# Optimization experiments

Measured on AMD Instinct MI355X. Metric: run time of the kernel, lower is better.

Reference implementation:

```python
import jax, jax.numpy as jnp
import numpy as np

N_NODES = 50000
N_EDGES = 800000
N_GRAPHS = 256
D_FEAT = 96
HIDDEN = 32


def setup_inputs() -> dict:
    key = jax.random.key(0)
    ks = jax.random.split(key, 8)
    x = jax.random.normal(ks[0], (N_NODES, D_FEAT), dtype=jnp.float32)
    edge_index = jax.random.randint(ks[1], (2, N_EDGES), 0, N_NODES, dtype=jnp.int64)
    batch = jnp.sort(jax.random.randint(ks[2], (N_NODES,), 0, N_GRAPHS, dtype=jnp.int64))
    W1 = jax.random.normal(ks[3], (D_FEAT, HIDDEN), dtype=jnp.float32) * 0.05
    b1 = jnp.zeros((HIDDEN,), dtype=jnp.float32)
    W2 = jax.random.normal(ks[4], (HIDDEN, HIDDEN), dtype=jnp.float32) * 0.05
    b2 = jnp.zeros((HIDDEN,), dtype=jnp.float32)
    Wc = jax.random.normal(ks[5], (HIDDEN, 2), dtype=jnp.float32) * 0.05
    bc = jnp.zeros((2,), dtype=jnp.float32)
    return {"x": x, "edge_index": edge_index, "batch": batch,
            "W1": W1, "b1": b1, "W2": W2, "b2": b2, "Wc": Wc, "bc": bc}


def reference(x, edge_index, batch, W1, b1, W2, b2, Wc, bc):
    src, dst = edge_index[0], edge_index[1]
    # GIN aggregation (eps=0): h_i = x_i + sum_{j -> i} x_j, scatter-add over edges
    agg = jax.ops.segment_sum(x[src], dst, num_segments=N_NODES)
    h = agg + x
    # 2-layer MLP inside GINConv
    h = jnp.maximum(h @ W1 + b1, 0.0) @ W2 + b2
    # outer ReLU (F.relu in forward)
    h = jnp.maximum(h, 0.0)
    # global mean pool per graph
    sums = jax.ops.segment_sum(h, batch, num_segments=N_GRAPHS)          # [G, H]
    counts = jax.ops.segment_sum(jnp.ones((N_NODES,), h.dtype), batch,
                                 num_segments=N_GRAPHS)                   # [G]
    pooled = sums / jnp.maximum(counts, 1.0)[:, None]
    return pooled @ Wc + bc  # [G, 2]
```

## Files before the change

### kernel.cpp

```cpp
#include <hip/hip_runtime.h>
#include <hip/hip_fp16.h>

#define N_NODES 50000
#define N_EDGES 800000
#define N_GRAPHS 256
#define D_FEAT 96
#define HIDDEN 32

#define NB 196
#define PB 500
#define PCHUNK 1600
#define SEGCAP 32
#define NLOAD 16
#define GWIN 16
#define LCAP 6400
#define XT 64
#define XBLK 782
#define XS_STRIDE 97
#define DUMMY_NODE N_NODES

__global__ void __launch_bounds__(256)
k_front(const float* __restrict__ x, const float* __restrict__ W1,
        __half* __restrict__ y16,
        const int* __restrict__ src, const int* __restrict__ dst,
        unsigned int* __restrict__ binned, unsigned short* __restrict__ cnt,
        float* __restrict__ sums, float* __restrict__ counts) {
    __shared__ __align__(16) char smem[26656];
    int blk = blockIdx.x;
    int tid = threadIdx.x;
    if (blk < PB) {
        int* hcur = (int*)smem;
        for (int i = tid; i < NB; i += 256) hcur[i] = 0;
        __syncthreads();

        int e0 = blk * PCHUNK, e1 = e0 + PCHUNK;
        for (int it = 0; it < PCHUNK; it += 1024) {
            int e = e0 + it + tid * 4;
            if (e < e1) {
                int4 s4 = *(const int4*)&src[e];
                int4 d4 = *(const int4*)&dst[e];
                unsigned w0 = (unsigned)s4.x | ((unsigned)(d4.x & 255) << 16);
                unsigned w1 = (unsigned)s4.y | ((unsigned)(d4.y & 255) << 16);
                unsigned w2 = (unsigned)s4.z | ((unsigned)(d4.z & 255) << 16);
                unsigned w3 = (unsigned)s4.w | ((unsigned)(d4.w & 255) << 16);
                int b0 = d4.x >> 8, b1 = d4.y >> 8, b2 = d4.z >> 8, b3 = d4.w >> 8;
                int p0 = atomicAdd(&hcur[b0], 1);
                int p1 = atomicAdd(&hcur[b1], 1);
                int p2 = atomicAdd(&hcur[b2], 1);
                int p3 = atomicAdd(&hcur[b3], 1);
                if (p0 < SEGCAP) binned[((size_t)b0 * PB + blk) * SEGCAP + p0] = w0;
                if (p1 < SEGCAP) binned[((size_t)b1 * PB + blk) * SEGCAP + p1] = w1;
                if (p2 < SEGCAP) binned[((size_t)b2 * PB + blk) * SEGCAP + p2] = w2;
                if (p3 < SEGCAP) binned[((size_t)b3 * PB + blk) * SEGCAP + p3] = w3;
            }
        }
        __syncthreads();

        for (int i = tid; i < NB; i += 256) {
            int c = hcur[i]; if (c > SEGCAP) c = SEGCAP;
            cnt[i * PB + blk] = (unsigned short)c;
        }
    } else {
        float* xs = (float*)smem;
        int xb = blk - PB;
        int n0 = xb * XT;
        int nn = N_NODES - n0; if (nn > XT) nn = XT;

        int gid = xb * 256 + tid;
        if (gid < N_GRAPHS * HIDDEN) sums[gid] = 0.f;
        if (gid < N_GRAPHS) counts[gid] = 0.f;
        if (xb == 0 && tid < HIDDEN)
            y16[(size_t)DUMMY_NODE * HIDDEN + tid] = __float2half(0.f);

        const float4* xsrc = (const float4*)(x + (size_t)n0 * D_FEAT);
        int nf4 = nn * (D_FEAT / 4);
        for (int idx = tid; idx < nf4; idx += 256) {
            int ln = (idx * 2731) >> 16;
            int k4 = idx - ln * 24;
            float4 v = xsrc[idx];
            float* dp = &xs[ln * XS_STRIDE + k4 * 4];
            dp[0] = v.x; dp[1] = v.y; dp[2] = v.z; dp[3] = v.w;
        }
        __syncthreads();

        int lane = tid & 63;
        int f0 = (tid >> 6) << 3;
        f0 = __builtin_amdgcn_readfirstlane(f0);

        if (lane < nn) {
            const float* xr = &xs[lane * XS_STRIDE];
            const float4* W1v = (const float4*)W1;
            float acc[8];
#pragma unroll
            for (int j = 0; j < 8; ++j) acc[j] = 0.f;
#pragma unroll
            for (int k = 0; k < D_FEAT; ++k) {
                float xv = xr[k];
                float4 wa = W1v[k * 8 + (f0 >> 2)];
                float4 wb = W1v[k * 8 + (f0 >> 2) + 1];
                acc[0] = fmaf(xv, wa.x, acc[0]);
                acc[1] = fmaf(xv, wa.y, acc[1]);
                acc[2] = fmaf(xv, wa.z, acc[2]);
                acc[3] = fmaf(xv, wa.w, acc[3]);
                acc[4] = fmaf(xv, wb.x, acc[4]);
                acc[5] = fmaf(xv, wb.y, acc[5]);
                acc[6] = fmaf(xv, wb.z, acc[6]);
                acc[7] = fmaf(xv, wb.w, acc[7]);
            }
            __half2 h01 = __floats2half2_rn(acc[0], acc[1]);
            __half2 h23 = __floats2half2_rn(acc[2], acc[3]);
            __half2 h45 = __floats2half2_rn(acc[4], acc[5]);
            __half2 h67 = __floats2half2_rn(acc[6], acc[7]);
            float4 pack;
            pack.x = __uint_as_float(*(const unsigned*)&h01);
            pack.y = __uint_as_float(*(const unsigned*)&h23);
            pack.z = __uint_as_float(*(const unsigned*)&h45);
            pack.w = __uint_as_float(*(const unsigned*)&h67);
            *(float4*)&y16[(size_t)(n0 + lane) * HIDDEN + f0] = pack;
        }
    }
}

__global__ void __launch_bounds__(1024)
k_agg(const unsigned int* __restrict__ binned, const unsigned short* __restrict__ cnt,
      const __half* __restrict__ y16, const int* __restrict__ batch,
      const float* __restrict__ b1, const float* __restrict__ W2,
      const float* __restrict__ b2,
      float* __restrict__ sums, float* __restrict__ counts) {
    __shared__ unsigned int list[LCAP];
    __shared__ unsigned short list2[LCAP];
    __shared__ unsigned int sA[512], sB[512];
    __shared__ unsigned short cs[PB];
    __shared__ unsigned int sOfs[PB];
    __shared__ unsigned int ncnt[256];
    __shared__ unsigned int offs[257];
    __shared__ unsigned int cur[256];
    __shared__ float w2s[HIDDEN * HIDDEN];
    __shared__ float accs[GWIN * HIDDEN];
    __shared__ float cntsl[GWIN];

    int tid = threadIdx.x;
    int bin = blockIdx.x;
    if (tid < 256) ncnt[tid] = 0;
    w2s[tid] = W2[tid];
    if (tid < GWIN * HIDDEN) accs[tid] = 0.f;
    if (tid < GWIN) cntsl[tid] = 0.f;
    if (tid < 512) {
        unsigned c = (tid < PB) ? (unsigned)cnt[bin * PB + tid] : 0u;
        if (tid < PB) cs[tid] = (unsigned short)c;
        sA[tid] = c;
    }

    const unsigned int* ebase = binned + (size_t)bin * PB * SEGCAP;
    unsigned u[NLOAD];
#pragma unroll
    for (int j = 0; j < NLOAD; ++j)
        u[j] = ebase[tid + j * 1024];
    __syncthreads();

    unsigned *ps = sA, *pd = sB;
    for (int d = 1; d < 512; d <<= 1) {
        if (tid < 512) { unsigned v = ps[tid]; if (tid >= d) v += ps[tid - d]; pd[tid] = v; }
        __syncthreads();
        unsigned* t = ps; ps = pd; pd = t;
    }
    if (tid < PB) sOfs[tid] = tid ? ps[tid - 1] : 0u;
    int ecount = (int)ps[PB - 1];
    if (ecount > LCAP) ecount = LCAP;
    __syncthreads();

#pragma unroll
    for (int j = 0; j < NLOAD; ++j) {
        int idx = tid + j * 1024;
        if (idx < PB * SEGCAP) {
            int s = idx >> 5;
            int i = idx & 31;
            if (i < (int)cs[s]) {
                unsigned pos = sOfs[s] + i;
                if (pos < LCAP) list[pos] = u[j];
            }
        }
    }
    __syncthreads();

    for (int e = tid; e < ecount; e += 1024)
        atomicAdd(&ncnt[list[e] >> 16], 1u);
    __syncthreads();

    if (tid < 256) sA[tid] = (ncnt[tid] + 7u) & ~7u;
    __syncthreads();
    ps = sA; pd = sB;
    for (int d = 1; d < 256; d <<= 1) {
        if (tid < 256) { unsigned v = ps[tid]; if (tid >= d) v += ps[tid - d]; pd[tid] = v; }
        __syncthreads();
        unsigned* t = ps; ps = pd; pd = t;
    }
    if (tid < 256) {
        offs[tid + 1] = ps[tid];
        cur[tid] = tid ? ps[tid - 1] : 0u;
    }
    if (tid == 0) offs[0] = 0;
    __syncthreads();

    for (int e = tid; e < ecount; e += 1024) {
        unsigned p = list[e];
        unsigned pos = atomicAdd(&cur[p >> 16], 1u);
        if (pos < LCAP) list2[pos] = (unsigned short)(p & 0xFFFFu);
    }
    __syncthreads();
    if (tid < 256) {
        unsigned i0 = cur[tid], i1 = offs[tid + 1];
        for (unsigned i = i0; i < i1 && i < LCAP; ++i)
            list2[i] = (unsigned short)DUMMY_NODE;
    }
    __syncthreads();

    int node0 = bin << 8;
    int nn = N_NODES - node0; if (nn > 256) nn = 256;
    int g = tid >> 5;
    int f = tid & 31;
    int gfirst = batch[node0];

    for (int ln = g * 8; ln < g * 8 + 8; ++ln) {
        if (ln >= nn) break;
        int node = node0 + ln;
        float acc = __half2float(y16[(size_t)node * HIDDEN + f]);
        int j = offs[ln], jend = offs[ln + 1];
        for (; j < jend; j += 8) {
            ushort4 qa = *(const ushort4*)&list2[j];
            ushort4 qb = *(const ushort4*)&list2[j + 4];
            float a0 = __half2float(y16[(size_t)qa.x * HIDDEN + f]);
            float a1 = __half2float(y16[(size_t)qa.y * HIDDEN + f]);
            float a2 = __half2float(y16[(size_t)qa.z * HIDDEN + f]);
            float a3 = __half2float(y16[(size_t)qa.w * HIDDEN + f]);
            float a4 = __half2float(y16[(size_t)qb.x * HIDDEN + f]);
            float a5 = __half2float(y16[(size_t)qb.y * HIDDEN + f]);
            float a6 = __half2float(y16[(size_t)qb.z * HIDDEN + f]);
            float a7 = __half2float(y16[(size_t)qb.w * HIDDEN + f]);
            acc += ((a0 + a1) + (a2 + a3)) + ((a4 + a5) + (a6 + a7));
        }

        float h1 = fmaxf(acc + b1[f], 0.f);
        float h2 = b2[f];
#pragma unroll
        for (int k = 0; k < HIDDEN; ++k)
            h2 = fmaf(__shfl(h1, k, 32), w2s[k * HIDDEN + f], h2);
        float h = fmaxf(h2, 0.f);

        int gr = batch[node];
        int b = gr - gfirst;
        if (b < GWIN) {
            atomicAdd(&accs[b * HIDDEN + f], h);
            if (f == 0) atomicAdd(&cntsl[b], 1.f);
        } else {
            atomicAdd(&sums[(size_t)gr * HIDDEN + f], h);
            if (f == 0) atomicAdd(&counts[gr], 1.f);
        }
    }
    __syncthreads();

    for (int i = tid; i < GWIN * HIDDEN; i += 1024) {
        float v = accs[i];
        if (v != 0.f) atomicAdd(&sums[(size_t)gfirst * HIDDEN + i], v);
    }
    if (tid < GWIN) {
        float c = cntsl[tid];
        if (c != 0.f) atomicAdd(&counts[gfirst + tid], c);
    }
}

__global__ void k_out(const float* __restrict__ sums, const float* __restrict__ counts,
                      const float* __restrict__ Wc, const float* __restrict__ bc,
                      float* __restrict__ out) {
    int g = threadIdx.x;
    if (g >= N_GRAPHS) return;
    float inv = 1.f / fmaxf(counts[g], 1.f);
    float o0 = bc[0], o1 = bc[1];
#pragma unroll
    for (int k = 0; k < HIDDEN; ++k) {
        float p = sums[(size_t)g * HIDDEN + k] * inv;
        o0 = fmaf(p, Wc[k * 2 + 0], o0);
        o1 = fmaf(p, Wc[k * 2 + 1], o1);
    }
    out[g * 2 + 0] = o0;
    out[g * 2 + 1] = o1;
}

extern "C" void kernel_launch(void* const* d_in, const int* in_sizes, int n_in,
                              void* d_out, int out_size, void* d_ws, size_t ws_size,
                              hipStream_t stream) {
    const float* x     = (const float*)d_in[0];
    const int*   ei    = (const int*)d_in[1];
    const int*   batch = (const int*)d_in[2];
    const float* W1    = (const float*)d_in[3];
    const float* b1    = (const float*)d_in[4];
    const float* W2    = (const float*)d_in[5];
    const float* b2    = (const float*)d_in[6];
    const float* Wc    = (const float*)d_in[7];
    const float* bc    = (const float*)d_in[8];
    float* out = (float*)d_out;

    char* ws = (char*)d_ws;
    float*          sums   = (float*)ws;
    float*          counts = (float*)(ws + 32768);
    unsigned short* cnt    = (unsigned short*)(ws + 33792);
    unsigned int*   binned = (unsigned int*)(ws + 229792);
    __half*         y16    = (__half*)(ws + 12773792);

    k_front<<<PB + XBLK, 256, 0, stream>>>(
        x, W1, y16, ei, ei + N_EDGES, binned, cnt, sums, counts);

    k_agg<<<NB, 1024, 0, stream>>>(binned, cnt, y16, batch,
                                   b1, W2, b2, sums, counts);

    k_out<<<1, 256, 0, stream>>>(sums, counts, Wc, bc, out);
}
```

Before: 127.0 us.

## Shrink aggregation bins to 64 nodes and drop intermediate edge compaction

Bins are shrunk from 256 to 64 destination nodes, so the aggregation kernel runs 782 blocks instead of 196. That fills more compute units and cuts per-block work and synchronisation. The old two-stage compaction (block-wide scan into a 32-bit list, then re-binning by node) is replaced by counting and scattering straight from registers, with a single wavefront shuffle scan over 64 node counts. The cost is a binned buffer twice the size (with SEGCAP 16) and more per-bin count entries, which adds memory traffic in both kernels.

```diff
diff --git a/kernel.cpp b/kernel.cpp
--- a/kernel.cpp
+++ b/kernel.cpp
@@ -7,13 +7,14 @@
 #define D_FEAT 96
 #define HIDDEN 32
 
-#define NB 196
+#define NB 782
+#define BN 64
 #define PB 500
 #define PCHUNK 1600
-#define SEGCAP 32
-#define NLOAD 16
-#define GWIN 16
-#define LCAP 6400
+#define SEGCAP 16
+#define NLOAD 8
+#define GWIN 4
+#define LCAP2 2048
 #define XT 64
 #define XBLK 782
 #define XS_STRIDE 97
@@ -43,7 +44,7 @@
                 unsigned w1 = (unsigned)s4.y | ((unsigned)(d4.y & 255) << 16);
                 unsigned w2 = (unsigned)s4.z | ((unsigned)(d4.z & 255) << 16);
                 unsigned w3 = (unsigned)s4.w | ((unsigned)(d4.w & 255) << 16);
-                int b0 = d4.x >> 8, b1 = d4.y >> 8, b2 = d4.z >> 8, b3 = d4.w >> 8;
+                int b0 = d4.x >> 6, b1 = d4.y >> 6, b2 = d4.z >> 6, b3 = d4.w >> 6;
                 int p0 = atomicAdd(&hcur[b0], 1);
                 int p1 = atomicAdd(&hcur[b1], 1);
                 int p2 = atomicAdd(&hcur[b2], 1);
@@ -127,105 +128,89 @@
       const float* __restrict__ b1, const float* __restrict__ W2,
       const float* __restrict__ b2,
       float* __restrict__ sums, float* __restrict__ counts) {
-    __shared__ unsigned int list[LCAP];
-    __shared__ unsigned short list2[LCAP];
-    __shared__ unsigned int sA[512], sB[512];
-    __shared__ unsigned short cs[PB];
-    __shared__ unsigned int sOfs[PB];
-    __shared__ unsigned int ncnt[256];
-    __shared__ unsigned int offs[257];
-    __shared__ unsigned int cur[256];
+    __shared__ unsigned short list2[LCAP2];
+    __shared__ unsigned short cs[512];
+    __shared__ unsigned int ncnt[BN];
+    __shared__ unsigned int offs[BN + 1];
+    __shared__ unsigned int cur[BN];
     __shared__ float w2s[HIDDEN * HIDDEN];
     __shared__ float accs[GWIN * HIDDEN];
     __shared__ float cntsl[GWIN];
 
     int tid = threadIdx.x;
     int bin = blockIdx.x;
-    if (tid < 256) ncnt[tid] = 0;
+
+    if (tid < BN) ncnt[tid] = 0;
     w2s[tid] = W2[tid];
     if (tid < GWIN * HIDDEN) accs[tid] = 0.f;
     if (tid < GWIN) cntsl[tid] = 0.f;
-    if (tid < 512) {
-        unsigned c = (tid < PB) ? (unsigned)cnt[bin * PB + tid] : 0u;
-        if (tid < PB) cs[tid] = (unsigned short)c;
-        sA[tid] = c;
-    }
+    if (tid < 512)
+        cs[tid] = (tid < PB) ? cnt[bin * PB + tid] : (unsigned short)0;
 
     const unsigned int* ebase = binned + (size_t)bin * PB * SEGCAP;
     unsigned u[NLOAD];
 #pragma unroll
-    for (int j = 0; j < NLOAD; ++j)
-        u[j] = ebase[tid + j * 1024];
-    __syncthreads();
-
-    unsigned *ps = sA, *pd = sB;
-    for (int d = 1; d < 512; d <<= 1) {
-        if (tid < 512) { unsigned v = ps[tid]; if (tid >= d) v += ps[tid - d]; pd[tid] = v; }
-        __syncthreads();
-        unsigned* t = ps; ps = pd; pd = t;
-    }
-    if (tid < PB) sOfs[tid] = tid ? ps[tid - 1] : 0u;
-    int ecount = (int)ps[PB - 1];
-    if (ecount > LCAP) ecount = LCAP;
-    __syncthreads();
-
-#pragma unroll
     for (int j = 0; j < NLOAD; ++j) {
         int idx = tid + j * 1024;
-        if (idx < PB * SEGCAP) {
-            int s = idx >> 5;
-            int i = idx & 31;
-            if (i < (int)cs[s]) {
-                unsigned pos = sOfs[s] + i;
-                if (pos < LCAP) list[pos] = u[j];
-            }
-        }
-    }
-    __syncthreads();
-
-    for (int e = tid; e < ecount; e += 1024)
-        atomicAdd(&ncnt[list[e] >> 16], 1u);
-    __syncthreads();
-
-    if (tid < 256) sA[tid] = (ncnt[tid] + 7u) & ~7u;
-    __syncthreads();
-    ps = sA; pd = sB;
-    for (int d = 1; d < 256; d <<= 1) {
-        if (tid < 256) { unsigned v = ps[tid]; if (tid >= d) v += ps[tid - d]; pd[tid] = v; }
-        __syncthreads();
-        unsigned* t = ps; ps = pd; pd = t;
-    }
-    if (tid < 256) {
-        offs[tid + 1] = ps[tid];
-        cur[tid] = tid ? ps[tid - 1] : 0u;
+        u[j] = (idx < PB * SEGCAP) ? ebase[idx] : 0u;
+    }
+    __syncthreads();
+
+#pragma unroll
+    for (int j = 0; j < NLOAD; ++j) {
+        int idx = tid + j * 1024;
+        int s = idx >> 4;
+        int i = idx & 15;
+        if (i < (int)cs[s])
+            atomicAdd(&ncnt[(u[j] >> 16) & 63], 1u);
+    }
+    __syncthreads();
+
+    if (tid < BN) {
+        unsigned pc = (ncnt[tid] + 7u) & ~7u;
+        unsigned v = pc;
+#pragma unroll
+        for (int d = 1; d < BN; d <<= 1) {
+            unsigned t = __shfl_up(v, d, 64);
+            if (tid >= d) v += t;
+        }
+        offs[tid + 1] = v;
+        cur[tid] = v - pc;
     }
     if (tid == 0) offs[0] = 0;
     __syncthreads();
 
-    for (int e = tid; e < ecount; e += 1024) {
-        unsigned p = list[e];
-        unsigned pos = atomicAdd(&cur[p >> 16], 1u);
-        if (pos < LCAP) list2[pos] = (unsigned short)(p & 0xFFFFu);
-    }
-    __syncthreads();
-    if (tid < 256) {
+#pragma unroll
+    for (int j = 0; j < NLOAD; ++j) {
+        int idx = tid + j * 1024;
+        int s = idx >> 4;
+        int i = idx & 15;
+        if (i < (int)cs[s]) {
+            unsigned p = u[j];
+            unsigned pos = atomicAdd(&cur[(p >> 16) & 63], 1u);
+            if (pos < LCAP2) list2[pos] = (unsigned short)(p & 0xFFFFu);
+        }
+    }
+    __syncthreads();
+    if (tid < BN) {
         unsigned i0 = cur[tid], i1 = offs[tid + 1];
-        for (unsigned i = i0; i < i1 && i < LCAP; ++i)
+        for (unsigned i = i0; i < i1 && i < LCAP2; ++i)
             list2[i] = (unsigned short)DUMMY_NODE;
     }
     __syncthreads();
 
-    int node0 = bin << 8;
-    int nn = N_NODES - node0; if (nn > 256) nn = 256;
+    int node0 = bin << 6;
+    int nn = N_NODES - node0; if (nn > BN) nn = BN;
     int g = tid >> 5;
     int f = tid & 31;
     int gfirst = batch[node0];
 
-    for (int ln = g * 8; ln < g * 8 + 8; ++ln) {
+    for (int ln = g * 2; ln < g * 2 + 2; ++ln) {
         if (ln >= nn) break;
         int node = node0 + ln;
         float acc = __half2float(y16[(size_t)node * HIDDEN + f]);
-        int j = offs[ln], jend = offs[ln + 1];
+        int j = offs[ln];
+        int jend = offs[ln + 1]; if (jend > LCAP2) jend = LCAP2;
         for (; j < jend; j += 8) {
             ushort4 qa = *(const ushort4*)&list2[j];
             ushort4 qb = *(const ushort4*)&list2[j + 4];
@@ -259,9 +244,9 @@
     }
     __syncthreads();
 
-    for (int i = tid; i < GWIN * HIDDEN; i += 1024) {
-        float v = accs[i];
-        if (v != 0.f) atomicAdd(&sums[(size_t)gfirst * HIDDEN + i], v);
+    if (tid < GWIN * HIDDEN) {
+        float v = accs[tid];
+        if (v != 0.f) atomicAdd(&sums[(size_t)gfirst * HIDDEN + tid], v);
     }
     if (tid < GWIN) {
         float c = cntsl[tid];
@@ -304,8 +289,8 @@
     float*          sums   = (float*)ws;
     float*          counts = (float*)(ws + 32768);
     unsigned short* cnt    = (unsigned short*)(ws + 33792);
-    unsigned int*   binned = (unsigned int*)(ws + 229792);
-    __half*         y16    = (__half*)(ws + 12773792);
+    unsigned int*   binned = (unsigned int*)(ws + 815792);
+    __half*         y16    = (__half*)(ws + 25839792);
 
     k_front<<<PB + XBLK, 256, 0, stream>>>(
         x, W1, y16, ei, ei + N_EDGES, binned, cnt, sums, counts);
```

Measured after the change: 140.0 us. +10.2%, slower.
